# Performance work log

Hardware: AMD Instinct MI355X
Metric: run time of the kernel (lower is better)

Reference implementation:

```python
import jax, jax.numpy as jnp
import numpy as np
from jax import lax

C = 64      # embed_dim
DI = 128    # d_inner (expand=2)
N = 16      # d_state
RK = 4      # dt_rank = ceil(C/16)
K = 4       # scan directions
NB = 8      # total VSS blocks (4 stages x 2)


def conv2d(x, w, b, stride=1, pad=1, groups=1):
    y = lax.conv_general_dilated(x, w, (stride, stride), [(pad, pad), (pad, pad)],
                                 dimension_numbers=('NCHW', 'OIHW', 'NCHW'),
                                 feature_group_count=groups)
    return y + b[None, :, None, None]


def ln2d(x, g, b, eps=1e-6):
    xt = x.transpose(0, 2, 3, 1)
    mu = xt.mean(-1, keepdims=True)
    var = ((xt - mu) ** 2).mean(-1, keepdims=True)
    y = (xt - mu) / jnp.sqrt(var + eps) * g + b
    return y.transpose(0, 3, 1, 2)


def selective_scan(u, delta, A, Bm, Cm, D):
    # u, delta: (B,K,d,L); A: (K,d,n); Bm, Cm: (B,K,n,L); D: (K,d)
    dA = jnp.exp(delta[..., None] * A[None, :, :, None, :])               # (B,K,d,L,n)
    dBu = delta[..., None] * Bm.transpose(0, 1, 3, 2)[:, :, None] * u[..., None]

    def comb(c1, c2):
        a1, b1 = c1
        a2, b2 = c2
        return a2 * a1, a2 * b1 + b2

    _, h = lax.associative_scan(comb, (dA, dBu), axis=3)                  # (B,K,d,L,n)
    y = jnp.einsum('bkdln,bkln->bkdl', h, Cm.transpose(0, 1, 3, 2))
    return y + D[None, :, :, None] * u


def vss_block(x, lg, lb, inw, cw, cb, xpw, dtw, dtb, a_log, dp, ong, onb, outw):
    B, _, H, W = x.shape
    L = H * W
    h = ln2d(x, lg, lb)
    xz = jnp.einsum('bchw,ce->behw', h, inw)                              # (B,2*DI,H,W)
    xc, z = xz[:, :DI], xz[:, DI:]
    xc = jax.nn.silu(conv2d(xc, cw, cb, groups=DI))                       # depthwise 3x3
    x1 = xc.reshape(B, DI, L)                                             # row-major
    x2 = xc.transpose(0, 1, 3, 2).reshape(B, DI, L)                       # col-major
    xs = jnp.stack([x1, x2, x1[..., ::-1], x2[..., ::-1]], axis=1)        # (B,K,DI,L)
    xdbl = jnp.einsum('bkdl,krd->bkrl', xs, xpw)
    dts, Bs, Cs = xdbl[:, :, :RK], xdbl[:, :, RK:RK + N], xdbl[:, :, RK + N:]
    delta = jax.nn.softplus(jnp.einsum('bkrl,kdr->bkdl', dts, dtw) + dtb[None, :, :, None])
    A = -jnp.exp(a_log)
    ys = selective_scan(xs, delta, A, Bs, Cs, dp)                         # (B,K,DI,L)
    y = (ys[:, 0].reshape(B, DI, H, W)
         + ys[:, 1].reshape(B, DI, W, H).transpose(0, 1, 3, 2)
         + ys[:, 2, :, ::-1].reshape(B, DI, H, W)
         + ys[:, 3, :, ::-1].reshape(B, DI, W, H).transpose(0, 1, 3, 2))
    yt = y.transpose(0, 2, 3, 1)
    mu = yt.mean(-1, keepdims=True)
    var = ((yt - mu) ** 2).mean(-1, keepdims=True)
    yt = (yt - mu) / jnp.sqrt(var + 1e-6) * ong + onb
    yt = yt * jax.nn.silu(z.transpose(0, 2, 3, 1))
    out = jnp.einsum('bhwd,dc->bhwc', yt, outw).transpose(0, 3, 1, 2)
    return x + out


def setup_inputs() -> dict:
    key = jax.random.key(0)
    ks = jax.random.split(key, 16)
    nrm = lambda k, s, sc=0.02: jax.random.normal(k, s, jnp.float32) * sc
    return dict(
        E0=jax.random.uniform(ks[0], (1, 1, 256, 256), jnp.float32),
        pe_w=nrm(ks[1], (C, 1, 4, 4), 0.1),
        pe_b=jnp.zeros((C,), jnp.float32),
        pe_lg=jnp.ones((C,), jnp.float32),
        pe_lb=jnp.zeros((C,), jnp.float32),
        ln_g=jnp.ones((NB, C), jnp.float32),
        ln_b=jnp.zeros((NB, C), jnp.float32),
        in_w=nrm(ks[2], (NB, C, 2 * DI)),
        cv_w=nrm(ks[3], (NB, DI, 1, 3, 3), 0.1),
        cv_b=jnp.zeros((NB, DI), jnp.float32),
        xp_w=nrm(ks[4], (NB, K, RK + 2 * N, DI)),
        dt_w=nrm(ks[5], (NB, K, DI, RK)),
        dt_b=nrm(ks[6], (NB, K, DI), 0.5),
        A_log=jnp.broadcast_to(jnp.log(jnp.arange(1., N + 1)), (NB, K, DI, N)).astype(jnp.float32),
        Dp=jnp.ones((NB, K, DI), jnp.float32),
        on_g=jnp.ones((NB, DI), jnp.float32),
        on_b=jnp.zeros((NB, DI), jnp.float32),
        out_pw=nrm(ks[7], (NB, DI, C)),
        dn_w=nrm(ks[8], (3, C, C, 3, 3), 0.05),
        dn_b=jnp.zeros((3, C), jnp.float32),
        dn_g=jnp.ones((3, C), jnp.float32),
        dn_lb=jnp.zeros((3, C), jnp.float32),
        up_w=nrm(ks[9], (3, C, C, 3, 3), 0.05),
        up_b=jnp.zeros((3, C), jnp.float32),
        oc_w=nrm(ks[10], (C, C, 3, 3), 0.05),
        oc_b=jnp.zeros((C,), jnp.float32),
    )


def reference(E0, pe_w, pe_b, pe_lg, pe_lb, ln_g, ln_b, in_w, cv_w, cv_b, xp_w,
              dt_w, dt_b, A_log, Dp, on_g, on_b, out_pw, dn_w, dn_b, dn_g, dn_lb,
              up_w, up_b, oc_w, oc_b):
    x = conv2d(E0, pe_w, pe_b, stride=4, pad=0)
    x = ln2d(x, pe_lg, pe_lb)
    skips = []
    cur = 0
    for i in range(4):
        for _ in range(2):
            x = vss_block(x, ln_g[cur], ln_b[cur], in_w[cur], cv_w[cur], cv_b[cur],
                          xp_w[cur], dt_w[cur], dt_b[cur], A_log[cur], Dp[cur],
                          on_g[cur], on_b[cur], out_pw[cur])
            cur += 1
        skips.append(x)
        if i < 3:
            x = ln2d(conv2d(x, dn_w[i], dn_b[i], stride=2), dn_g[i], dn_lb[i])
    for i in range(3):
        Bq, Cq, Hq, Wq = x.shape
        x = jax.image.resize(x, (Bq, Cq, Hq * 2, Wq * 2), method='bilinear')
        x = jax.nn.silu(conv2d(x, up_w[i], up_b[i]))
        x = x + skips[-(i + 2)]
    Bq, Cq, Hq, Wq = x.shape
    x = jax.image.resize(x, (Bq, Cq, Hq * 4, Wq * 4), method='bilinear')
    x = jax.nn.silu(conv2d(x, oc_w, oc_b))
    return x
```

## Files before the change

kernel.cpp:

```cpp
#include <hip/hip_runtime.h>
#include <hip/hip_bf16.h>
#include <utility>

#define CIC 8

__global__ void k_patch_embed_ln(const float* __restrict__ E0, const float* __restrict__ w,
                                 const float* __restrict__ b, const float* __restrict__ g,
                                 const float* __restrict__ lb, float* __restrict__ out) {
  int p = blockIdx.x;
  int c = threadIdx.x;
  int oh = p >> 6, ow = p & 63;
  const float* src = E0 + (oh * 4) * 256 + ow * 4;
  const float* wc = w + c * 16;
  float acc = b[c];
#pragma unroll
  for (int i = 0; i < 4; i++)
#pragma unroll
    for (int j = 0; j < 4; j++) acc += src[i * 256 + j] * wc[i * 4 + j];
  float s = acc, s2 = acc * acc;
#pragma unroll
  for (int m = 32; m >= 1; m >>= 1) {
    s += __shfl_xor(s, m, 64);
    s2 += __shfl_xor(s2, m, 64);
  }
  float mu = s * (1.f / 64.f);
  float var = s2 * (1.f / 64.f) - mu * mu;
  float rstd = rsqrtf(var + 1e-6f);
  out[c * 4096 + p] = (acc - mu) * rstd * g[c] + lb[c];
}

__global__ void k_ln2d64(const float* __restrict__ x, const float* __restrict__ g,
                         const float* __restrict__ b, float* __restrict__ y, int HW) {
  int p = blockIdx.x;
  int c = threadIdx.x;
  float v = x[c * HW + p];
  float s = v, s2 = v * v;
#pragma unroll
  for (int m = 32; m >= 1; m >>= 1) {
    s += __shfl_xor(s, m, 64);
    s2 += __shfl_xor(s2, m, 64);
  }
  float mu = s * (1.f / 64.f);
  float var = s2 * (1.f / 64.f) - mu * mu;
  float rstd = rsqrtf(var + 1e-6f);
  y[c * HW + p] = (v - mu) * rstd * g[c] + b[c];
}

__global__ void k_lnproj(const float* __restrict__ x, const float* __restrict__ g,
                         const float* __restrict__ b, const float* __restrict__ w,
                         float* __restrict__ xc, float* __restrict__ z, int HW) {
  int p = blockIdx.x;
  int t = threadIdx.x;
  __shared__ float hsh[64];
  if (t < 64) {
    float v = x[t * HW + p];
    float s = v, s2 = v * v;
#pragma unroll
    for (int m = 32; m >= 1; m >>= 1) {
      s += __shfl_xor(s, m, 64);
      s2 += __shfl_xor(s2, m, 64);
    }
    float mu = s * (1.f / 64.f);
    float var = s2 * (1.f / 64.f) - mu * mu;
    float rstd = rsqrtf(var + 1e-6f);
    hsh[t] = (v - mu) * rstd * g[t] + b[t];
  }
  __syncthreads();
  float acc = 0.f;
  const float* wp = w + t;
#pragma unroll
  for (int c = 0; c < 64; c++) acc += hsh[c] * wp[c * 256];
  if (t < 128)
    xc[(size_t)p * 128 + t] = acc;
  else
    z[(size_t)p * 128 + (t - 128)] = acc;
}

__global__ void k_dwconv(const float* __restrict__ xc, const float* __restrict__ w,
                         const float* __restrict__ b, float* __restrict__ out, int H, int lgH) {
  int HW = H * H;
  int idx = blockIdx.x * blockDim.x + threadIdx.x;
  if (idx >= 128 * HW) return;
  int p = idx >> 7;
  int d = idx & 127;
  int ph = p >> lgH, pw = p & (H - 1);
  const float* wp = w + d * 9;
  float acc = b[d];
#pragma unroll
  for (int i = 0; i < 3; i++) {
    int ih = ph + i - 1;
    if (ih < 0 || ih >= H) continue;
#pragma unroll
    for (int j = 0; j < 3; j++) {
      int iw = pw + j - 1;
      if (iw < 0 || iw >= H) continue;
      acc += xc[(size_t)(ih * H + iw) * 128 + d] * wp[i * 3 + j];
    }
  }
  out[(size_t)p * 128 + d] = acc / (1.f + __expf(-acc));
}

__global__ void k_xproj(const float* __restrict__ xcs, const float* __restrict__ xpw,
                        const float* __restrict__ dtw, const float* __restrict__ dtb,
                        float* __restrict__ delta, float* __restrict__ Bs,
                        float* __restrict__ Cs, int H, int lgH) {
  int L = H * H;
  int l = blockIdx.x;
  int k = blockIdx.y;
  int t = threadIdx.x;
  int lm = (k & 2) ? (L - 1 - l) : l;
  int idx = (k & 1) ? ((lm & (H - 1)) * H + (lm >> lgH)) : lm;
  __shared__ float xs[128];
  __shared__ float part[36][4];
  __shared__ float r4[4];
  if (t < 128) xs[t] = xcs[(size_t)idx * 128 + t];
  __syncthreads();
  if (t < 144) {
    int r = t >> 2, q = t & 3;
    const float* wr = xpw + (k * 36 + r) * 128 + q * 32;
    const float* xp = xs + q * 32;
    float acc = 0.f;
#pragma unroll
    for (int c = 0; c < 32; c++) acc += xp[c] * wr[c];
    part[r][q] = acc;
  }
  __syncthreads();
  if (t < 36) {
    float acc = part[t][0] + part[t][1] + part[t][2] + part[t][3];
    if (t < 4)
      r4[t] = acc;
    else if (t < 20)
      Bs[((size_t)k * L + l) * 16 + (t - 4)] = acc;
    else
      Cs[((size_t)k * L + l) * 16 + (t - 20)] = acc;
  }
  __syncthreads();
  if (t < 128) {
    float dt = dtb[k * 128 + t];
    const float* wd = dtw + (k * 128 + t) * 4;
    dt += r4[0] * wd[0] + r4[1] * wd[1] + r4[2] * wd[2] + r4[3] * wd[3];
    float sp = fmaxf(dt, 0.f) + log1pf(__expf(-fabsf(dt)));
    delta[((size_t)k * L + l) * 128 + t] = sp;
  }
}

__global__ void k_scanA(const float* __restrict__ xcs, const float* __restrict__ delta,
                        const float* __restrict__ Bs, const float* __restrict__ A_log,
                        float* __restrict__ hloc, float* __restrict__ pA, int H, int lgH,
                        int nc, int cs) {
  int L = H * H;
  int c = blockIdx.x;
  int k = blockIdx.y;
  int d = threadIdx.x;
  float A[16], h[16];
#pragma unroll
  for (int n = 0; n < 16; n++) {
    A[n] = -expf(A_log[(k * 128 + d) * 16 + n]);
    h[n] = 0.f;
  }
  float sumdt = 0.f;
  int l0 = c * cs;
  for (int l = l0; l < l0 + cs; l++) {
    int lm = (k & 2) ? (L - 1 - l) : l;
    int idx = (k & 1) ? ((lm & (H - 1)) * H + (lm >> lgH)) : lm;
    float u = xcs[(size_t)idx * 128 + d];
    float dt = delta[((size_t)k * L + l) * 128 + d];
    float du = dt * u;
    sumdt += dt;
    const float4* bp = (const float4*)(Bs + ((size_t)k * L + l) * 16);
    float4 B0 = bp[0], B1 = bp[1], B2 = bp[2], B3 = bp[3];
    float Bv[16] = {B0.x, B0.y, B0.z, B0.w, B1.x, B1.y, B1.z, B1.w,
                    B2.x, B2.y, B2.z, B2.w, B3.x, B3.y, B3.z, B3.w};
#pragma unroll
    for (int n = 0; n < 16; n++) h[n] = __expf(dt * A[n]) * h[n] + Bv[n] * du;
  }
  size_t base = (((size_t)(k * 128 + d)) * nc + c) * 16;
#pragma unroll
  for (int n = 0; n < 16; n++) {
    hloc[base + n] = h[n];
    pA[base + n] = __expf(A[n] * sumdt);
  }
}

__global__ void k_scanB(const float* __restrict__ hloc, const float* __restrict__ pA,
                        float* __restrict__ hinit, int nc) {
  int tid = blockIdx.x * blockDim.x + threadIdx.x;
  int k = tid >> 11;
  int d = (tid >> 4) & 127;
  int n = tid & 15;
  size_t rb = ((size_t)(k * 128 + d)) * nc * 16 + n;
  float h = 0.f;
  for (int c = 0; c < nc; c++) {
    size_t a = rb + (size_t)c * 16;
    hinit[a] = h;
    h = pA[a] * h + hloc[a];
  }
}

__global__ void k_scanC(const float* __restrict__ xcs, const float* __restrict__ delta,
                        const float* __restrict__ Bs, const float* __restrict__ Cs,
                        const float* __restrict__ A_log, const float* __restrict__ Dp,
                        const float* __restrict__ hinit, float* __restrict__ ys, int H,
                        int lgH, int nc, int cs) {
  int L = H * H;
  int c = blockIdx.x;
  int k = blockIdx.y;
  int d = threadIdx.x;
  float A[16], h[16];
  size_t base = (((size_t)(k * 128 + d)) * nc + c) * 16;
#pragma unroll
  for (int n = 0; n < 16; n++) {
    A[n] = -expf(A_log[(k * 128 + d) * 16 + n]);
    h[n] = hinit[base + n];
  }
  float Dv = Dp[k * 128 + d];
  int l0 = c * cs;
  for (int l = l0; l < l0 + cs; l++) {
    int lm = (k & 2) ? (L - 1 - l) : l;
    int idx = (k & 1) ? ((lm & (H - 1)) * H + (lm >> lgH)) : lm;
    float u = xcs[(size_t)idx * 128 + d];
    float dt = delta[((size_t)k * L + l) * 128 + d];
    float du = dt * u;
    const float4* bp = (const float4*)(Bs + ((size_t)k * L + l) * 16);
    float4 B0 = bp[0], B1 = bp[1], B2 = bp[2], B3 = bp[3];
    float Bv[16] = {B0.x, B0.y, B0.z, B0.w, B1.x, B1.y, B1.z, B1.w,
                    B2.x, B2.y, B2.z, B2.w, B3.x, B3.y, B3.z, B3.w};
    const float4* cp = (const float4*)(Cs + ((size_t)k * L + l) * 16);
    float4 C0 = cp[0], C1 = cp[1], C2 = cp[2], C3 = cp[3];
    float Cv[16] = {C0.x, C0.y, C0.z, C0.w, C1.x, C1.y, C1.z, C1.w,
                    C2.x, C2.y, C2.z, C2.w, C3.x, C3.y, C3.z, C3.w};
    float y = 0.f;
#pragma unroll
    for (int n = 0; n < 16; n++) {
      h[n] = __expf(dt * A[n]) * h[n] + Bv[n] * du;
      y += h[n] * Cv[n];
    }
    ys[((size_t)k * L + l) * 128 + d] = y + Dv * u;
  }
}

__global__ void k_combine(const float* __restrict__ ys, const float* __restrict__ z,
                          const float* __restrict__ xin, const float* __restrict__ ong,
                          const float* __restrict__ onb, const float* __restrict__ outw,
                          float* __restrict__ xout, int H, int lgH) {
  int L = H * H;
  int p = blockIdx.x;
  int d = threadIdx.x;
  int ph = p >> lgH, pw = p & (H - 1);
  int l1 = pw * H + ph;
  float yv = ys[((size_t)0 * L + p) * 128 + d] + ys[((size_t)1 * L + l1) * 128 + d] +
             ys[((size_t)2 * L + (L - 1 - p)) * 128 + d] +
             ys[((size_t)3 * L + (L - 1 - l1)) * 128 + d];
  float s = yv, s2 = yv * yv;
#pragma unroll
  for (int m = 32; m >= 1; m >>= 1) {
    s += __shfl_xor(s, m, 64);
    s2 += __shfl_xor(s2, m, 64);
  }
  __shared__ float ws1[2], ws2[2];
  int wid = d >> 6;
  if ((d & 63) == 0) {
    ws1[wid] = s;
    ws2[wid] = s2;
  }
  __syncthreads();
  float tot = ws1[0] + ws1[1], tot2 = ws2[0] + ws2[1];
  float mu = tot * (1.f / 128.f);
  float var = tot2 * (1.f / 128.f) - mu * mu;
  float rstd = rsqrtf(var + 1e-6f);
  float zt = z[(size_t)p * 128 + d];
  float yt = ((yv - mu) * rstd * ong[d] + onb[d]) * (zt / (1.f + __expf(-zt)));
  __shared__ float ysm[128];
  ysm[d] = yt;
  __syncthreads();
  if (d < 64) {
    float acc = xin[(size_t)d * L + p];
#pragma unroll
    for (int q = 0; q < 128; q++) acc += ysm[q] * outw[q * 64 + d];
    xout[(size_t)d * L + p] = acc;
  }
}

__global__ void k_conv_naive(const float* __restrict__ x, const float* __restrict__ w,
                             const float* __restrict__ b, const float* __restrict__ skip,
                             float* __restrict__ out, int Hin, int Hout, int stride,
                             int do_silu) {
  int idx = blockIdx.x * blockDim.x + threadIdx.x;
  int HWo = Hout * Hout;
  if (idx >= 64 * HWo) return;
  int co = idx / HWo;
  int p = idx - co * HWo;
  int oh = p / Hout, ow = p - (p / Hout) * Hout;
  float acc = b[co];
  const float* wb = w + co * 64 * 9;
  for (int ci = 0; ci < 64; ci++) {
    const float* xb = x + (size_t)ci * Hin * Hin;
    const float* wc = wb + ci * 9;
#pragma unroll
    for (int i = 0; i < 3; i++) {
      int ih = oh * stride + i - 1;
      if (ih < 0 || ih >= Hin) continue;
#pragma unroll
      for (int j = 0; j < 3; j++) {
        int iw = ow * stride + j - 1;
        if (iw < 0 || iw >= Hin) continue;
        acc += xb[ih * Hin + iw] * wc[i * 3 + j];
      }
    }
  }
  if (do_silu) acc = acc / (1.f + __expf(-acc));
  if (skip) acc += skip[idx];
  out[idx] = acc;
}

__global__ void __launch_bounds__(256) k_conv16(const float* __restrict__ x,
                                                const float* __restrict__ w,
                                                const float* __restrict__ b,
                                                float* __restrict__ out, int H, int W,
                                                int do_silu) {
  __shared__ __align__(16) float xsh[CIC][18][18];
  __shared__ __align__(16) float wsh[CIC][64][12];
  int t = threadIdx.x;
  int q = t & 63, cog = t >> 6;
  int qx = q & 7, qy = q >> 3;
  int ox = blockIdx.x * 16, oy = blockIdx.y * 16;
  float acc[4][16];
#pragma unroll
  for (int pp = 0; pp < 4; pp++)
#pragma unroll
    for (int i = 0; i < 16; i++) acc[pp][i] = 0.f;
  for (int cb = 0; cb < 64; cb += CIC) {
    for (int i = t; i < CIC * 324; i += 256) {
      int ci = i / 324;
      int r = i - ci * 324;
      int iy = r / 18, ix = r - (r / 18) * 18;
      int gy = oy + iy - 1, gx = ox + ix - 1;
      float v = 0.f;
      if (gy >= 0 && gy < H && gx >= 0 && gx < W) v = x[(size_t)(cb + ci) * H * W + gy * W + gx];
      xsh[ci][iy][ix] = v;
    }
    for (int i = t; i < CIC * 576; i += 256) {
      int ci = i / 576;
      int r = i - ci * 576;
      int co = r / 9, tap = r - (r / 9) * 9;
      wsh[ci][co][tap] = w[(size_t)co * 576 + (cb + ci) * 9 + tap];
    }
    __syncthreads();
#pragma unroll
    for (int ci = 0; ci < CIC; ci++) {
      float xv[4][4];
#pragma unroll
      for (int r = 0; r < 4; r++) {
        float2 a = *(const float2*)&xsh[ci][2 * qy + r][2 * qx];
        float2 bq = *(const float2*)&xsh[ci][2 * qy + r][2 * qx + 2];
        xv[r][0] = a.x;
        xv[r][1] = a.y;
        xv[r][2] = bq.x;
        xv[r][3] = bq.y;
      }
#pragma unroll
      for (int i = 0; i < 16; i++) {
        int co = cog * 16 + i;
        float4 w0 = *(const float4*)&wsh[ci][co][0];
        float4 w1 = *(const float4*)&wsh[ci][co][4];
        float w8 = wsh[ci][co][8];
#pragma unroll
        for (int dy = 0; dy < 2; dy++)
#pragma unroll
          for (int dx = 0; dx < 2; dx++) {
            float* a = acc[dy * 2 + dx];
            a[i] += xv[dy + 0][dx + 0] * w0.x + xv[dy + 0][dx + 1] * w0.y +
                    xv[dy + 0][dx + 2] * w0.z + xv[dy + 1][dx + 0] * w0.w +
                    xv[dy + 1][dx + 1] * w1.x + xv[dy + 1][dx + 2] * w1.y +
                    xv[dy + 2][dx + 0] * w1.z + xv[dy + 2][dx + 1] * w1.w +
                    xv[dy + 2][dx + 2] * w8;
          }
      }
    }
    __syncthreads();
  }
#pragma unroll
  for (int dy = 0; dy < 2; dy++)
#pragma unroll
    for (int dx = 0; dx < 2; dx++) {
      int gy = oy + 2 * qy + dy, gx = ox + 2 * qx + dx;
#pragma unroll
      for (int i = 0; i < 16; i++) {
        float a = acc[dy * 2 + dx][i] + b[cog * 16 + i];
        if (do_silu) a = a / (1.f + __expf(-a));
        out[(size_t)(cog * 16 + i) * H * W + gy * W + gx] = a;
      }
    }
}

__global__ void k_resize(const float* __restrict__ x, float* __restrict__ out, int Hin,
                         int Win, int Hout, int Wout, float inv_scale) {
  int idx = blockIdx.x * blockDim.x + threadIdx.x;
  int HWo = Hout * Wout;
  if (idx >= 64 * HWo) return;
  int c = idx / HWo;
  int p = idx - c * HWo;
  int oh = p / Wout, ow = p - (p / Wout) * Wout;
  float sh = (oh + 0.5f) * inv_scale - 0.5f;
  float sw = (ow + 0.5f) * inv_scale - 0.5f;
  int h0 = (int)floorf(sh);
  float fh = sh - h0;
  int w0 = (int)floorf(sw);
  float fw = sw - w0;
  int h0c = min(max(h0, 0), Hin - 1), h1c = min(max(h0 + 1, 0), Hin - 1);
  int w0c = min(max(w0, 0), Win - 1), w1c = min(max(w0 + 1, 0), Win - 1);
  const float* xb = x + (size_t)c * Hin * Win;
  float v = (1.f - fh) * ((1.f - fw) * xb[h0c * Win + w0c] + fw * xb[h0c * Win + w1c]) +
            fh * ((1.f - fw) * xb[h1c * Win + w0c] + fw * xb[h1c * Win + w1c]);
  out[idx] = v;
}

extern "C" void kernel_launch(void* const* d_in, const int* in_sizes, int n_in, void* d_out,
                              int out_size, void* d_ws, size_t ws_size, hipStream_t stream) {
  const float* E0 = (const float*)d_in[0];
  const float* pe_w = (const float*)d_in[1];
  const float* pe_b = (const float*)d_in[2];
  const float* pe_lg = (const float*)d_in[3];
  const float* pe_lb = (const float*)d_in[4];
  const float* ln_g = (const float*)d_in[5];
  const float* ln_b = (const float*)d_in[6];
  const float* in_w = (const float*)d_in[7];
  const float* cv_w = (const float*)d_in[8];
  const float* cv_b = (const float*)d_in[9];
  const float* xp_w = (const float*)d_in[10];
  const float* dt_w = (const float*)d_in[11];
  const float* dt_b = (const float*)d_in[12];
  const float* A_log = (const float*)d_in[13];
  const float* Dp = (const float*)d_in[14];
  const float* on_g = (const float*)d_in[15];
  const float* on_b = (const float*)d_in[16];
  const float* out_pw = (const float*)d_in[17];
  const float* dn_w = (const float*)d_in[18];
  const float* dn_b = (const float*)d_in[19];
  const float* dn_g = (const float*)d_in[20];
  const float* dn_lb = (const float*)d_in[21];
  const float* up_w = (const float*)d_in[22];
  const float* up_b = (const float*)d_in[23];
  const float* oc_w = (const float*)d_in[24];
  const float* oc_b = (const float*)d_in[25];

  float* ws = (float*)d_ws;
  size_t off = 0;
  auto alloc = [&](size_t n) {
    float* p = ws + off;
    off += n;
    return p;
  };
  float* xA = alloc(64 * 4096);
  float* xB = alloc(64 * 4096);
  float* xc = alloc(128 * 4096);
  float* zb = alloc(128 * 4096);
  float* xcs = alloc(128 * 4096);
  float* dlt = alloc((size_t)4 * 128 * 4096);
  float* Bsb = alloc(4 * 16 * 4096);
  float* Csb = alloc(4 * 16 * 4096);
  float* ysb = alloc((size_t)4 * 128 * 4096);
  float* hloc = alloc((size_t)4 * 128 * 128 * 16);
  float* pAb = alloc((size_t)4 * 128 * 128 * 16);
  float* hin = alloc((size_t)4 * 128 * 128 * 16);
  float* sk0 = alloc(64 * 4096);
  float* sk1 = alloc(64 * 1024);
  float* sk2 = alloc(64 * 256);
  float* sk3 = alloc(64 * 64);
  float* tmpR = alloc((size_t)64 * 256 * 256);

  k_patch_embed_ln<<<4096, 64, 0, stream>>>(E0, pe_w, pe_b, pe_lg, pe_lb, xB);
  float* x = xB;
  float* xalt = xA;

  int Hs[4] = {64, 32, 16, 8};
  int lgHs[4] = {6, 5, 4, 3};
  int CSs[4] = {32, 16, 8, 8};
  float* skips[4] = {sk0, sk1, sk2, sk3};
  int cur = 0;

  auto vss = [&](int H, int lgH, int cs) {
    int L = H * H;
    int nc = L / cs;
    k_lnproj<<<L, 256, 0, stream>>>(x, ln_g + cur * 64, ln_b + cur * 64,
                                    in_w + (size_t)cur * 64 * 256, xc, zb, L);
    k_dwconv<<<(128 * L + 255) / 256, 256, 0, stream>>>(xc, cv_w + (size_t)cur * 128 * 9,
                                                        cv_b + cur * 128, xcs, H, lgH);
    dim3 gx(L, 4);
    k_xproj<<<gx, 256, 0, stream>>>(xcs, xp_w + (size_t)cur * 4 * 36 * 128,
                                    dt_w + (size_t)cur * 4 * 128 * 4, dt_b + cur * 4 * 128,
                                    dlt, Bsb, Csb, H, lgH);
    dim3 ga(nc, 4);
    k_scanA<<<ga, 128, 0, stream>>>(xcs, dlt, Bsb, A_log + (size_t)cur * 4 * 128 * 16, hloc,
                                    pAb, H, lgH, nc, cs);
    k_scanB<<<32, 256, 0, stream>>>(hloc, pAb, hin, nc);
    k_scanC<<<ga, 128, 0, stream>>>(xcs, dlt, Bsb, Csb, A_log + (size_t)cur * 4 * 128 * 16,
                                    Dp + cur * 4 * 128, hin, ysb, H, lgH, nc, cs);
    k_combine<<<L, 128, 0, stream>>>(ysb, zb, x, on_g + cur * 128, on_b + cur * 128,
                                     out_pw + (size_t)cur * 128 * 64, xalt, H, lgH);
    std::swap(x, xalt);
    cur++;
  };

  for (int i = 0; i < 4; i++) {
    int H = Hs[i], lgH = lgHs[i];
    vss(H, lgH, CSs[i]);
    vss(H, lgH, CSs[i]);
    hipMemcpyAsync(skips[i], x, (size_t)64 * H * H * sizeof(float),
                   hipMemcpyDeviceToDevice, stream);
    if (i < 3) {
      int Ho = H / 2;
      k_conv_naive<<<(64 * Ho * Ho + 255) / 256, 256, 0, stream>>>(
          x, dn_w + (size_t)i * 64 * 64 * 9, dn_b + i * 64, nullptr, xalt, H, Ho, 2, 0);
      k_ln2d64<<<Ho * Ho, 64, 0, stream>>>(xalt, dn_g + i * 64, dn_lb + i * 64, x, Ho * Ho);
    }
  }

  for (int i = 0; i < 3; i++) {
    int Hin = 8 << i, Ho = Hin * 2;
    k_resize<<<(64 * Ho * Ho + 255) / 256, 256, 0, stream>>>(x, tmpR, Hin, Hin, Ho, Ho, 0.5f);
    k_conv_naive<<<(64 * Ho * Ho + 255) / 256, 256, 0, stream>>>(
        tmpR, up_w + (size_t)i * 64 * 64 * 9, up_b + i * 64, skips[2 - i], xalt, Ho, Ho, 1, 1);
    std::swap(x, xalt);
  }

  k_resize<<<(64 * 256 * 256 + 255) / 256, 256, 0, stream>>>(x, tmpR, 64, 64, 256, 256, 0.25f);
  dim3 gf(16, 16);
  k_conv16<<<gf, 256, 0, stream>>>(tmpR, oc_w, oc_b, (float*)d_out, 256, 256, 1);
}
```

Measured before the change: 1.314 ms.

## Fuse scan stages, combine with next lnproj, and resize into final conv

Adds a single-launch, per-direction fused scan kernel (chunk-local pass, carry propagation, output pass) for the small stages. It also fuses the first block's combine with the second block's LayerNorm and in-projection, and folds the final 4x bilinear upsample into the output conv. That final conv is split across output-channel groups for more blocks with fewer accumulators per thread. Scan chunk sizes are halved for the first two stages. These changes remove kernel launches and the large 256x256 intermediate buffer, at the cost of recomputing interpolation per tile load and running only 4 blocks for the fused scan.

```diff
diff --git a/kernel.cpp b/kernel.cpp
--- a/kernel.cpp
+++ b/kernel.cpp
@@ -239,6 +239,94 @@
   }
 }
 
+__global__ void __launch_bounds__(1024) k_scan_fused(
+    const float* __restrict__ xcs, const float* __restrict__ delta,
+    const float* __restrict__ Bs, const float* __restrict__ Cs,
+    const float* __restrict__ A_log, const float* __restrict__ Dp,
+    float* __restrict__ hloc, float* __restrict__ pA, float* __restrict__ hinit,
+    float* __restrict__ ys, int H, int lgH, int nc) {
+  const int cs = 8;
+  int L = H * H;
+  int k = blockIdx.x;
+  for (int item = threadIdx.x; item < nc * 128; item += 1024) {
+    int c = item >> 7, d = item & 127;
+    float A[16], h[16];
+#pragma unroll
+    for (int n = 0; n < 16; n++) {
+      A[n] = -expf(A_log[(k * 128 + d) * 16 + n]);
+      h[n] = 0.f;
+    }
+    float sumdt = 0.f;
+    int l0 = c * cs;
+    for (int l = l0; l < l0 + cs; l++) {
+      int lm = (k & 2) ? (L - 1 - l) : l;
+      int idx = (k & 1) ? ((lm & (H - 1)) * H + (lm >> lgH)) : lm;
+      float u = xcs[(size_t)idx * 128 + d];
+      float dt = delta[((size_t)k * L + l) * 128 + d];
+      float du = dt * u;
+      sumdt += dt;
+      const float4* bp = (const float4*)(Bs + ((size_t)k * L + l) * 16);
+      float4 B0 = bp[0], B1 = bp[1], B2 = bp[2], B3 = bp[3];
+      float Bv[16] = {B0.x, B0.y, B0.z, B0.w, B1.x, B1.y, B1.z, B1.w,
+                      B2.x, B2.y, B2.z, B2.w, B3.x, B3.y, B3.z, B3.w};
+#pragma unroll
+      for (int n = 0; n < 16; n++) h[n] = __expf(dt * A[n]) * h[n] + Bv[n] * du;
+    }
+    size_t base = (((size_t)(k * 128 + d)) * nc + c) * 16;
+#pragma unroll
+    for (int n = 0; n < 16; n++) {
+      hloc[base + n] = h[n];
+      pA[base + n] = __expf(A[n] * sumdt);
+    }
+  }
+  __syncthreads();
+  for (int item = threadIdx.x; item < 2048; item += 1024) {
+    int d = item >> 4, n = item & 15;
+    size_t rb = ((size_t)(k * 128 + d)) * nc * 16 + n;
+    float h = 0.f;
+    for (int c = 0; c < nc; c++) {
+      size_t a = rb + (size_t)c * 16;
+      hinit[a] = h;
+      h = pA[a] * h + hloc[a];
+    }
+  }
+  __syncthreads();
+  for (int item = threadIdx.x; item < nc * 128; item += 1024) {
+    int c = item >> 7, d = item & 127;
+    float A[16], h[16];
+    size_t base = (((size_t)(k * 128 + d)) * nc + c) * 16;
+#pragma unroll
+    for (int n = 0; n < 16; n++) {
+      A[n] = -expf(A_log[(k * 128 + d) * 16 + n]);
+      h[n] = hinit[base + n];
+    }
+    float Dv = Dp[k * 128 + d];
+    int l0 = c * cs;
+    for (int l = l0; l < l0 + cs; l++) {
+      int lm = (k & 2) ? (L - 1 - l) : l;
+      int idx = (k & 1) ? ((lm & (H - 1)) * H + (lm >> lgH)) : lm;
+      float u = xcs[(size_t)idx * 128 + d];
+      float dt = delta[((size_t)k * L + l) * 128 + d];
+      float du = dt * u;
+      const float4* bp = (const float4*)(Bs + ((size_t)k * L + l) * 16);
+      float4 B0 = bp[0], B1 = bp[1], B2 = bp[2], B3 = bp[3];
+      float Bv[16] = {B0.x, B0.y, B0.z, B0.w, B1.x, B1.y, B1.z, B1.w,
+                      B2.x, B2.y, B2.z, B2.w, B3.x, B3.y, B3.z, B3.w};
+      const float4* cp = (const float4*)(Cs + ((size_t)k * L + l) * 16);
+      float4 C0 = cp[0], C1 = cp[1], C2 = cp[2], C3 = cp[3];
+      float Cv[16] = {C0.x, C0.y, C0.z, C0.w, C1.x, C1.y, C1.z, C1.w,
+                      C2.x, C2.y, C2.z, C2.w, C3.x, C3.y, C3.z, C3.w};
+      float y = 0.f;
+#pragma unroll
+      for (int n = 0; n < 16; n++) {
+        h[n] = __expf(dt * A[n]) * h[n] + Bv[n] * du;
+        y += h[n] * Cv[n];
+      }
+      ys[((size_t)k * L + l) * 128 + d] = y + Dv * u;
+    }
+  }
+}
+
 __global__ void k_combine(const float* __restrict__ ys, const float* __restrict__ z,
                           const float* __restrict__ xin, const float* __restrict__ ong,
                           const float* __restrict__ onb, const float* __restrict__ outw,
@@ -279,6 +367,73 @@
     for (int q = 0; q < 128; q++) acc += ysm[q] * outw[q * 64 + d];
     xout[(size_t)d * L + p] = acc;
   }
+}
+
+__global__ void k_combine_lnproj(const float* __restrict__ ys, const float* __restrict__ z,
+                                 const float* __restrict__ xin, const float* __restrict__ ong,
+                                 const float* __restrict__ onb, const float* __restrict__ outw,
+                                 const float* __restrict__ g2, const float* __restrict__ b2,
+                                 const float* __restrict__ w2, float* __restrict__ xout,
+                                 float* __restrict__ xc, float* __restrict__ zout, int H,
+                                 int lgH) {
+  int L = H * H;
+  int p = blockIdx.x;
+  int t = threadIdx.x;
+  __shared__ float ysm[128], hnsh[64];
+  __shared__ float ws1[2], ws2[2];
+  float yv = 0.f;
+  if (t < 128) {
+    int ph = p >> lgH, pw = p & (H - 1);
+    int l1 = pw * H + ph;
+    yv = ys[((size_t)0 * L + p) * 128 + t] + ys[((size_t)1 * L + l1) * 128 + t] +
+         ys[((size_t)2 * L + (L - 1 - p)) * 128 + t] +
+         ys[((size_t)3 * L + (L - 1 - l1)) * 128 + t];
+    float s = yv, s2 = yv * yv;
+#pragma unroll
+    for (int m = 32; m >= 1; m >>= 1) {
+      s += __shfl_xor(s, m, 64);
+      s2 += __shfl_xor(s2, m, 64);
+    }
+    if ((t & 63) == 0) {
+      ws1[t >> 6] = s;
+      ws2[t >> 6] = s2;
+    }
+  }
+  __syncthreads();
+  if (t < 128) {
+    float tot = ws1[0] + ws1[1], tot2 = ws2[0] + ws2[1];
+    float mu = tot * (1.f / 128.f);
+    float var = tot2 * (1.f / 128.f) - mu * mu;
+    float rstd = rsqrtf(var + 1e-6f);
+    float zt = z[(size_t)p * 128 + t];
+    ysm[t] = ((yv - mu) * rstd * ong[t] + onb[t]) * (zt / (1.f + __expf(-zt)));
+  }
+  __syncthreads();
+  if (t < 64) {
+    float acc = xin[(size_t)t * L + p];
+#pragma unroll
+    for (int q = 0; q < 128; q++) acc += ysm[q] * outw[q * 64 + t];
+    xout[(size_t)t * L + p] = acc;
+    float s = acc, s2 = acc * acc;
+#pragma unroll
+    for (int m = 32; m >= 1; m >>= 1) {
+      s += __shfl_xor(s, m, 64);
+      s2 += __shfl_xor(s2, m, 64);
+    }
+    float mu = s * (1.f / 64.f);
+    float var = s2 * (1.f / 64.f) - mu * mu;
+    float rstd = rsqrtf(var + 1e-6f);
+    hnsh[t] = (acc - mu) * rstd * g2[t] + b2[t];
+  }
+  __syncthreads();
+  float a2 = 0.f;
+  const float* wp = w2 + t;
+#pragma unroll
+  for (int c = 0; c < 64; c++) a2 += hnsh[c] * wp[c * 256];
+  if (t < 128)
+    xc[(size_t)p * 128 + t] = a2;
+  else
+    zout[(size_t)p * 128 + (t - 128)] = a2;
 }
 
 __global__ void k_conv_naive(const float* __restrict__ x, const float* __restrict__ w,
@@ -313,22 +468,22 @@
   out[idx] = acc;
 }
 
-__global__ void __launch_bounds__(256) k_conv16(const float* __restrict__ x,
-                                                const float* __restrict__ w,
-                                                const float* __restrict__ b,
-                                                float* __restrict__ out, int H, int W,
-                                                int do_silu) {
+__global__ void __launch_bounds__(256) k_conv16_up(const float* __restrict__ x,
+                                                   const float* __restrict__ w,
+                                                   const float* __restrict__ b,
+                                                   float* __restrict__ out) {
   __shared__ __align__(16) float xsh[CIC][18][18];
-  __shared__ __align__(16) float wsh[CIC][64][12];
+  __shared__ __align__(16) float wsh[CIC][16][12];
   int t = threadIdx.x;
   int q = t & 63, cog = t >> 6;
   int qx = q & 7, qy = q >> 3;
   int ox = blockIdx.x * 16, oy = blockIdx.y * 16;
-  float acc[4][16];
+  int z16 = blockIdx.z * 16;
+  float acc[4][4];
 #pragma unroll
   for (int pp = 0; pp < 4; pp++)
 #pragma unroll
-    for (int i = 0; i < 16; i++) acc[pp][i] = 0.f;
+    for (int i = 0; i < 4; i++) acc[pp][i] = 0.f;
   for (int cb = 0; cb < 64; cb += CIC) {
     for (int i = t; i < CIC * 324; i += 256) {
       int ci = i / 324;
@@ -336,14 +491,26 @@
       int iy = r / 18, ix = r - (r / 18) * 18;
       int gy = oy + iy - 1, gx = ox + ix - 1;
       float v = 0.f;
-      if (gy >= 0 && gy < H && gx >= 0 && gx < W) v = x[(size_t)(cb + ci) * H * W + gy * W + gx];
+      if (gy >= 0 && gy < 256 && gx >= 0 && gx < 256) {
+        float sh = gy * 0.25f - 0.375f;
+        float sw = gx * 0.25f - 0.375f;
+        int h0 = (int)floorf(sh);
+        float fh = sh - h0;
+        int w0 = (int)floorf(sw);
+        float fw = sw - w0;
+        int h0c = max(h0, 0), h1c = min(h0 + 1, 63);
+        int w0c = max(w0, 0), w1c = min(w0 + 1, 63);
+        const float* xb = x + (size_t)(cb + ci) * 4096;
+        v = (1.f - fh) * ((1.f - fw) * xb[h0c * 64 + w0c] + fw * xb[h0c * 64 + w1c]) +
+            fh * ((1.f - fw) * xb[h1c * 64 + w0c] + fw * xb[h1c * 64 + w1c]);
+      }
       xsh[ci][iy][ix] = v;
     }
-    for (int i = t; i < CIC * 576; i += 256) {
-      int ci = i / 576;
-      int r = i - ci * 576;
-      int co = r / 9, tap = r - (r / 9) * 9;
-      wsh[ci][co][tap] = w[(size_t)co * 576 + (cb + ci) * 9 + tap];
+    for (int i = t; i < CIC * 144; i += 256) {
+      int ci = i / 144;
+      int r = i - ci * 144;
+      int col = r / 9, tap = r - (r / 9) * 9;
+      wsh[ci][col][tap] = w[(size_t)(z16 + col) * 576 + (cb + ci) * 9 + tap];
     }
     __syncthreads();
 #pragma unroll
@@ -359,21 +526,20 @@
         xv[r][3] = bq.y;
       }
 #pragma unroll
-      for (int i = 0; i < 16; i++) {
-        int co = cog * 16 + i;
-        float4 w0 = *(const float4*)&wsh[ci][co][0];
-        float4 w1 = *(const float4*)&wsh[ci][co][4];
-        float w8 = wsh[ci][co][8];
+      for (int i = 0; i < 4; i++) {
+        int col = cog * 4 + i;
+        float4 w0 = *(const float4*)&wsh[ci][col][0];
+        float4 w1 = *(const float4*)&wsh[ci][col][4];
+        float w8 = wsh[ci][col][8];
 #pragma unroll
         for (int dy = 0; dy < 2; dy++)
 #pragma unroll
           for (int dx = 0; dx < 2; dx++) {
-            float* a = acc[dy * 2 + dx];
-            a[i] += xv[dy + 0][dx + 0] * w0.x + xv[dy + 0][dx + 1] * w0.y +
-                    xv[dy + 0][dx + 2] * w0.z + xv[dy + 1][dx + 0] * w0.w +
-                    xv[dy + 1][dx + 1] * w1.x + xv[dy + 1][dx + 2] * w1.y +
-                    xv[dy + 2][dx + 0] * w1.z + xv[dy + 2][dx + 1] * w1.w +
-                    xv[dy + 2][dx + 2] * w8;
+            acc[dy * 2 + dx][i] += xv[dy + 0][dx + 0] * w0.x + xv[dy + 0][dx + 1] * w0.y +
+                                   xv[dy + 0][dx + 2] * w0.z + xv[dy + 1][dx + 0] * w0.w +
+                                   xv[dy + 1][dx + 1] * w1.x + xv[dy + 1][dx + 2] * w1.y +
+                                   xv[dy + 2][dx + 0] * w1.z + xv[dy + 2][dx + 1] * w1.w +
+                                   xv[dy + 2][dx + 2] * w8;
           }
       }
     }
@@ -385,10 +551,11 @@
     for (int dx = 0; dx < 2; dx++) {
       int gy = oy + 2 * qy + dy, gx = ox + 2 * qx + dx;
 #pragma unroll
-      for (int i = 0; i < 16; i++) {
-        float a = acc[dy * 2 + dx][i] + b[cog * 16 + i];
-        if (do_silu) a = a / (1.f + __expf(-a));
-        out[(size_t)(cog * 16 + i) * H * W + gy * W + gx] = a;
+      for (int i = 0; i < 4; i++) {
+        int co = z16 + cog * 4 + i;
+        float a = acc[dy * 2 + dx][i] + b[co];
+        a = a / (1.f + __expf(-a));
+        out[(size_t)co * 65536 + gy * 256 + gx] = a;
       }
     }
 }
@@ -460,14 +627,14 @@
   float* Bsb = alloc(4 * 16 * 4096);
   float* Csb = alloc(4 * 16 * 4096);
   float* ysb = alloc((size_t)4 * 128 * 4096);
-  float* hloc = alloc((size_t)4 * 128 * 128 * 16);
-  float* pAb = alloc((size_t)4 * 128 * 128 * 16);
-  float* hin = alloc((size_t)4 * 128 * 128 * 16);
+  float* hloc = alloc((size_t)4 * 128 * 256 * 16);
+  float* pAb = alloc((size_t)4 * 128 * 256 * 16);
+  float* hin = alloc((size_t)4 * 128 * 256 * 16);
   float* sk0 = alloc(64 * 4096);
   float* sk1 = alloc(64 * 1024);
   float* sk2 = alloc(64 * 256);
   float* sk3 = alloc(64 * 64);
-  float* tmpR = alloc((size_t)64 * 256 * 256);
+  float* tmpR = alloc((size_t)64 * 4096);
 
   k_patch_embed_ln<<<4096, 64, 0, stream>>>(E0, pe_w, pe_b, pe_lg, pe_lb, xB);
   float* x = xB;
@@ -475,39 +642,53 @@
 
   int Hs[4] = {64, 32, 16, 8};
   int lgHs[4] = {6, 5, 4, 3};
-  int CSs[4] = {32, 16, 8, 8};
+  int CSs[4] = {16, 8, 8, 8};
   float* skips[4] = {sk0, sk1, sk2, sk3};
   int cur = 0;
 
-  auto vss = [&](int H, int lgH, int cs) {
+  auto vss_core = [&](int H, int lgH, int cs, bool fused_scan) {
     int L = H * H;
     int nc = L / cs;
-    k_lnproj<<<L, 256, 0, stream>>>(x, ln_g + cur * 64, ln_b + cur * 64,
-                                    in_w + (size_t)cur * 64 * 256, xc, zb, L);
     k_dwconv<<<(128 * L + 255) / 256, 256, 0, stream>>>(xc, cv_w + (size_t)cur * 128 * 9,
                                                         cv_b + cur * 128, xcs, H, lgH);
     dim3 gx(L, 4);
     k_xproj<<<gx, 256, 0, stream>>>(xcs, xp_w + (size_t)cur * 4 * 36 * 128,
                                     dt_w + (size_t)cur * 4 * 128 * 4, dt_b + cur * 4 * 128,
                                     dlt, Bsb, Csb, H, lgH);
-    dim3 ga(nc, 4);
-    k_scanA<<<ga, 128, 0, stream>>>(xcs, dlt, Bsb, A_log + (size_t)cur * 4 * 128 * 16, hloc,
-                                    pAb, H, lgH, nc, cs);
-    k_scanB<<<32, 256, 0, stream>>>(hloc, pAb, hin, nc);
-    k_scanC<<<ga, 128, 0, stream>>>(xcs, dlt, Bsb, Csb, A_log + (size_t)cur * 4 * 128 * 16,
-                                    Dp + cur * 4 * 128, hin, ysb, H, lgH, nc, cs);
+    const float* Al = A_log + (size_t)cur * 4 * 128 * 16;
+    const float* Dv = Dp + cur * 4 * 128;
+    if (fused_scan) {
+      k_scan_fused<<<4, 1024, 0, stream>>>(xcs, dlt, Bsb, Csb, Al, Dv, hloc, pAb, hin, ysb,
+                                           H, lgH, nc);
+    } else {
+      dim3 ga(nc, 4);
+      k_scanA<<<ga, 128, 0, stream>>>(xcs, dlt, Bsb, Al, hloc, pAb, H, lgH, nc, cs);
+      k_scanB<<<32, 256, 0, stream>>>(hloc, pAb, hin, nc);
+      k_scanC<<<ga, 128, 0, stream>>>(xcs, dlt, Bsb, Csb, Al, Dv, hin, ysb, H, lgH, nc, cs);
+    }
+  };
+
+  for (int i = 0; i < 4; i++) {
+    int H = Hs[i], lgH = lgHs[i];
+    int L = H * H;
+    bool fs = (i >= 2);
+    k_lnproj<<<L, 256, 0, stream>>>(x, ln_g + cur * 64, ln_b + cur * 64,
+                                    in_w + (size_t)cur * 64 * 256, xc, zb, L);
+    vss_core(H, lgH, CSs[i], fs);
+    k_combine_lnproj<<<L, 256, 0, stream>>>(
+        ysb, zb, x, on_g + cur * 128, on_b + cur * 128, out_pw + (size_t)cur * 128 * 64,
+        ln_g + (cur + 1) * 64, ln_b + (cur + 1) * 64, in_w + (size_t)(cur + 1) * 64 * 256,
+        xalt, xc, zb, H, lgH);
+    std::swap(x, xalt);
+    cur++;
+    vss_core(H, lgH, CSs[i], fs);
     k_combine<<<L, 128, 0, stream>>>(ysb, zb, x, on_g + cur * 128, on_b + cur * 128,
                                      out_pw + (size_t)cur * 128 * 64, xalt, H, lgH);
     std::swap(x, xalt);
     cur++;
-  };
-
-  for (int i = 0; i < 4; i++) {
-    int H = Hs[i], lgH = lgHs[i];
-    vss(H, lgH, CSs[i]);
-    vss(H, lgH, CSs[i]);
-    hipMemcpyAsync(skips[i], x, (size_t)64 * H * H * sizeof(float),
-                   hipMemcpyDeviceToDevice, stream);
+
+    hipMemcpyAsync(skips[i], x, (size_t)64 * L * sizeof(float), hipMemcpyDeviceToDevice,
+                   stream);
     if (i < 3) {
       int Ho = H / 2;
       k_conv_naive<<<(64 * Ho * Ho + 255) / 256, 256, 0, stream>>>(
@@ -524,7 +705,6 @@
     std::swap(x, xalt);
   }
 
-  k_resize<<<(64 * 256 * 256 + 255) / 256, 256, 0, stream>>>(x, tmpR, 64, 64, 256, 256, 0.25f);
-  dim3 gf(16, 16);
-  k_conv16<<<gf, 256, 0, stream>>>(tmpR, oc_w, oc_b, (float*)d_out, 256, 256, 1);
-}
+  dim3 gf(16, 16, 4);
+  k_conv16_up<<<gf, 256, 0, stream>>>(x, oc_w, oc_b, (float*)d_out);
+}
```

New measurement: 1.508 ms. +14.8%, slower.
